# Optimization experiments

Measured on AMD Instinct MI355X. Metric: run time of the kernel, lower is better.

## Reference

```python
import jax, jax.numpy as jnp
import numpy as np

M, T, D, H = 2, 2048, 1024, 16
HD = D // H
SCALE = 1.0 / np.sqrt(D).astype(np.float32)  # original divides by sqrt(emb_dim)


def setup_inputs() -> dict:
    key = jax.random.key(0)
    ks = jax.random.split(key, 8)
    def lin(k):
        kw, kb = jax.random.split(k)
        W = jax.random.normal(kw, (D, D), dtype=jnp.float32) * (1.0 / np.sqrt(D))
        b = jax.random.normal(kb, (D,), dtype=jnp.float32) * 0.01
        return W, b
    Wq, bq = lin(ks[0]); Wk, bk = lin(ks[1]); Wv, bv = lin(ks[2]); Wo, bo = lin(ks[3])
    Q = jax.random.normal(ks[4], (M, T, D), dtype=jnp.float32)
    K = jax.random.normal(ks[5], (M, T, D), dtype=jnp.float32)
    V = jax.random.normal(ks[6], (M, T, D), dtype=jnp.float32)
    mask = jnp.ones((M, 1, 1, T), dtype=jnp.int32)
    return {"Q": Q, "K": K, "V": V, "mask": mask,
            "Wq": Wq, "bq": bq, "Wk": Wk, "bk": bk,
            "Wv": Wv, "bv": bv, "Wo": Wo, "bo": bo}


def reference(Q, K, V, mask, Wq, bq, Wk, bk, Wv, bv, Wo, bo):
    m = Q.shape[0]
    # torch nn.Linear: y = x @ W.T + b
    q = (Q @ Wq.T + bq).reshape(m, -1, H, HD)  # (m, Tq, h, hd)
    k = (K @ Wk.T + bk).reshape(m, -1, H, HD)
    v = (V @ Wv.T + bv).reshape(m, -1, H, HD)
    energy = jnp.einsum('mqhd,mkhd->mhqk', q, k) * SCALE
    if mask is not None:
        energy = jnp.where(mask == 0, jnp.float32(-1e20), energy)
    attn = jax.nn.softmax(energy, axis=3)  # dropout is identity at inference
    out = jnp.einsum('mhqk,mkhd->mqhd', attn, v)  # (m, Tq, h, hd)
    concat = out.reshape(m, -1, H * HD)
    return concat @ Wo.T + bo
```

## Files before the change

kernel.cpp:

```cpp
#include <hip/hip_runtime.h>
#include <cstdint>
#include <cstddef>

#define T_SEQ 2048
#define D_EMB 1024
#define H_HEADS 16
#define MROWS 4096
#define SC2 (0.03125f * 1.44269504f)
#define MASKNEG (-1e30f)

typedef __attribute__((ext_vector_type(8))) short bf16x8;
typedef __attribute__((ext_vector_type(4))) float f32x4;
typedef __attribute__((ext_vector_type(16))) float f32x16;
typedef __attribute__((ext_vector_type(4))) unsigned short us4;

__device__ __forceinline__ unsigned short f2bf(float f) {
  union { float f; uint32_t u; } v; v.f = f;
  uint32_t u = v.u;
  return (unsigned short)((u + 0x7FFFu + ((u >> 16) & 1u)) >> 16);
}

__device__ __forceinline__ uint32_t cvtpk(float lo, float hi) {
  uint32_t r;
  asm("v_cvt_pk_bf16_f32 %0, %1, %2" : "=v"(r) : "v"(lo), "v"(hi));
  return r;
}

__device__ __forceinline__ float fexp2(float x) {
  float r;
  asm("v_exp_f32 %0, %1" : "=v"(r) : "v"(x));
  return r;
}

__device__ __forceinline__ float bf2f(unsigned short u) {
  union { uint32_t u; float f; } v; v.u = ((uint32_t)u) << 16;
  return v.f;
}

__device__ __forceinline__ void gl16(const void* g, void* l) {
  __builtin_amdgcn_global_load_lds(
      (const __attribute__((address_space(1))) unsigned int*)g,
      (__attribute__((address_space(3))) unsigned int*)l, 16, 0, 0);
}

__global__ __launch_bounds__(256) void cvt_all(
    const float* __restrict__ Q, const float* __restrict__ K, const float* __restrict__ V,
    const float* __restrict__ Wq, const float* __restrict__ Wk,
    const float* __restrict__ Wv, const float* __restrict__ Wo,
    unsigned short* __restrict__ Qb, unsigned short* __restrict__ Kb,
    unsigned short* __restrict__ Vb,
    unsigned short* __restrict__ Wqb, unsigned short* __restrict__ Wkb,
    unsigned short* __restrict__ Wvb, unsigned short* __restrict__ Wob) {
  int i = blockIdx.x * 256 + threadIdx.x;
  const float* src;
  unsigned short* dst;
  int j;
  if (i < 3145728) {
    int s = i >> 20;
    j = i & 1048575;
    src = (s == 0) ? Q : (s == 1) ? K : V;
    dst = (s == 0) ? Qb : (s == 1) ? Kb : Vb;
  } else {
    int k = i - 3145728;
    int s = k >> 18;
    j = k & 262143;
    src = (s == 0) ? Wq : (s == 1) ? Wk : (s == 2) ? Wv : Wo;
    dst = (s == 0) ? Wqb : (s == 1) ? Wkb : (s == 2) ? Wvb : Wob;
  }
  float4 f = ((const float4*)src)[j];
  us4 o;
  o[0] = f2bf(f.x); o[1] = f2bf(f.y); o[2] = f2bf(f.z); o[3] = f2bf(f.w);
  ((us4*)dst)[j] = o;
}

__global__ __launch_bounds__(256) void qkv_gemm(
    const unsigned short* __restrict__ Qb, const unsigned short* __restrict__ Kb,
    const unsigned short* __restrict__ Vb,
    const unsigned short* __restrict__ Wqb, const unsigned short* __restrict__ Wkb,
    const unsigned short* __restrict__ Wvb,
    const float* __restrict__ bq, const float* __restrict__ bk, const float* __restrict__ bv,
    unsigned short* __restrict__ qo, unsigned short* __restrict__ ko,
    unsigned short* __restrict__ vto) {
  const int swz = (blockIdx.x & 7) * 192 + (blockIdx.x >> 3);
  const int bx = swz & 15, by = (swz >> 4) & 31, z = swz >> 9;
  const unsigned short* A = (z == 0) ? Qb : (z == 1) ? Kb : Vb;
  const unsigned short* W = (z == 0) ? Wqb : (z == 1) ? Wkb : Wvb;
  const float* bias = (z == 0) ? bq : (z == 1) ? bk : bv;

  __shared__ __align__(16) unsigned short Asm[2][128 * 32];
  __shared__ __align__(16) unsigned short Bsm[2][64 * 32];

  const int tid = threadIdx.x;
  const int lane = tid & 63, w = tid >> 6;
  const int fq = lane >> 4, fr = lane & 15;
  const int brow = by * 128, bcol = bx * 64;
  const int wr = w * 32;

  f32x4 acc[2][4] = {};

#define QKV_STAGE(buf, k0)                                                     \
  {                                                                            \
    _Pragma("unroll") for (int it = 0; it < 2; ++it) {                         \
      int idx = it * 256 + tid;                                                \
      int row = idx >> 2, ce = (idx & 3) * 8;                                  \
      gl16(&A[(size_t)(brow + row) * D_EMB + (k0) + ce],                       \
           (char*)Asm[buf] + idx * 16);                                        \
    }                                                                          \
    {                                                                          \
      int row = tid >> 2, ce = (tid & 3) * 8;                                  \
      gl16(&W[(size_t)(bcol + row) * D_EMB + (k0) + ce],                       \
           (char*)Bsm[buf] + tid * 16);                                        \
    }                                                                          \
  }

#define QKV_COMPUTE(buf)                                                       \
  {                                                                            \
    bf16x8 af[2], bfr[4];                                                      \
    _Pragma("unroll") for (int i = 0; i < 2; ++i)                              \
        af[i] = *(const bf16x8*)((const char*)Asm[buf] +                       \
                                 (wr + i * 16 + fr) * 64 + fq * 16);           \
    _Pragma("unroll") for (int j = 0; j < 4; ++j)                              \
        bfr[j] = *(const bf16x8*)((const char*)Bsm[buf] +                      \
                                  (j * 16 + fr) * 64 + fq * 16);               \
    _Pragma("unroll") for (int i = 0; i < 2; ++i)                              \
        _Pragma("unroll") for (int j = 0; j < 4; ++j)                          \
            acc[i][j] = __builtin_amdgcn_mfma_f32_16x16x32_bf16(               \
                af[i], bfr[j], acc[i][j], 0, 0, 0);                            \
  }

  QKV_STAGE(0, 0);
  __syncthreads();
#pragma unroll 1
  for (int t = 0; t < 32; t += 2) {
    QKV_STAGE(1, (t + 1) * 32);
    QKV_COMPUTE(0);
    __syncthreads();
    if (t + 2 < 32) QKV_STAGE(0, (t + 2) * 32);
    QKV_COMPUTE(1);
    __syncthreads();
  }

#pragma unroll
  for (int i = 0; i < 2; ++i) {
#pragma unroll
    for (int j = 0; j < 4; ++j) {
      int r0 = brow + wr + i * 16 + fq * 4;
      int cc = bcol + j * 16 + fr;
      float bb = bias[cc];
      if (z < 2) {
        unsigned short* O = (z == 0) ? qo : ko;
        float sc = (z == 0) ? SC2 : 1.0f;
#pragma unroll
        for (int q = 0; q < 4; ++q)
          O[(size_t)(r0 + q) * D_EMB + cc] = f2bf((acc[i][j][q] + bb) * sc);
      } else {
        int hh = cc >> 6, dd = cc & 63;
        int mm = r0 >> 11, tt = r0 & 2047;
        us4 pk;
#pragma unroll
        for (int q = 0; q < 4; ++q) pk[q] = f2bf(acc[i][j][q] + bb);
        *(us4*)&vto[((size_t)((mm * H_HEADS + hh) * 64 + dd)) * T_SEQ + tt] = pk;
      }
    }
  }
}

__global__ __launch_bounds__(256) void out_gemm(const unsigned short* __restrict__ Ab,
                                                const unsigned short* __restrict__ Wb,
                                                const float* __restrict__ bias,
                                                float* __restrict__ Out) {
  const int swz = (blockIdx.x & 7) * 64 + (blockIdx.x >> 3);
  const int bx = swz & 15, by = swz >> 4;

  __shared__ __align__(16) unsigned short Asm[2][128 * 32];
  __shared__ __align__(16) unsigned short Bsm[2][64 * 32];
  const int tid = threadIdx.x;
  const int lane = tid & 63, w = tid >> 6;
  const int fq = lane >> 4, fr = lane & 15;
  const int brow = by * 128, bcol = bx * 64;
  const int wr = w * 32;

  f32x4 acc[2][4] = {};

#define OUT_STAGE(buf, k0)                                                     \
  {                                                                            \
    _Pragma("unroll") for (int it = 0; it < 2; ++it) {                         \
      int idx = it * 256 + tid;                                                \
      int row = idx >> 2, ce = (idx & 3) * 8;                                  \
      gl16(&Ab[(size_t)(brow + row) * D_EMB + (k0) + ce],                      \
           (char*)Asm[buf] + idx * 16);                                        \
    }                                                                          \
    {                                                                          \
      int row = tid >> 2, ce = (tid & 3) * 8;                                  \
      gl16(&Wb[(size_t)(bcol + row) * D_EMB + (k0) + ce],                      \
           (char*)Bsm[buf] + tid * 16);                                        \
    }                                                                          \
  }

#define OUT_COMPUTE(buf)                                                       \
  {                                                                            \
    bf16x8 af[2], bfr[4];                                                      \
    _Pragma("unroll") for (int i = 0; i < 2; ++i)                              \
        af[i] = *(const bf16x8*)((const char*)Asm[buf] +                       \
                                 (wr + i * 16 + fr) * 64 + fq * 16);           \
    _Pragma("unroll") for (int j = 0; j < 4; ++j)                              \
        bfr[j] = *(const bf16x8*)((const char*)Bsm[buf] +                      \
                                  (j * 16 + fr) * 64 + fq * 16);               \
    _Pragma("unroll") for (int i = 0; i < 2; ++i)                              \
        _Pragma("unroll") for (int j = 0; j < 4; ++j)                          \
            acc[i][j] = __builtin_amdgcn_mfma_f32_16x16x32_bf16(               \
                af[i], bfr[j], acc[i][j], 0, 0, 0);                            \
  }

  OUT_STAGE(0, 0);
  __syncthreads();
#pragma unroll 1
  for (int t = 0; t < 32; t += 2) {
    OUT_STAGE(1, (t + 1) * 32);
    OUT_COMPUTE(0);
    __syncthreads();
    if (t + 2 < 32) OUT_STAGE(0, (t + 2) * 32);
    OUT_COMPUTE(1);
    __syncthreads();
  }

#pragma unroll
  for (int i = 0; i < 2; ++i)
#pragma unroll
    for (int j = 0; j < 4; ++j) {
      int r0 = brow + wr + i * 16 + fq * 4;
      int cc = bcol + j * 16 + fr;
      float bb = bias[cc];
#pragma unroll
      for (int q = 0; q < 4; ++q)
        Out[(size_t)(r0 + q) * D_EMB + cc] = acc[i][j][q] + bb;
    }
}

__global__ __launch_bounds__(256, 4) void attn_fwd(const unsigned short* __restrict__ qb,
                                                   const unsigned short* __restrict__ kb,
                                                   const unsigned short* __restrict__ vtb,
                                                   const int* __restrict__ maskg,
                                                   unsigned short* __restrict__ opart,
                                                   float* __restrict__ lipart) {
  const int swzb = (blockIdx.x & 7) * 128 + (blockIdx.x >> 3);
  const int qt = swzb & 15, h = (swzb >> 4) & 15, mI = (swzb >> 8) & 1, sp = swzb >> 9;
  const int tid = threadIdx.x;
  const int lane = tid & 63, w = tid >> 6;
  const int lq = lane & 31, h2 = lane >> 5;
  const int xk = (lq & 7) << 4;
  const int vx = (lq & 7) << 4;

  __shared__ __align__(16) unsigned short Ksm[128 * 64];
  __shared__ __align__(16) unsigned short Vsm[64 * 128];
  __shared__ __align__(16) float Msm[128];
  __shared__ int moks[16];

  char* KsmB = (char*)Ksm;
  char* VsmB = (char*)Vsm;

  if (tid < 16) moks[tid] = 1;
  __syncthreads();
  {
    int bad = 0;
    const int4* mg = (const int4*)&maskg[mI * T_SEQ + tid * 8];
    int4 a = mg[0], b = mg[1];
    bad |= (a.x == 0) | (a.y == 0) | (a.z == 0) | (a.w == 0);
    bad |= (b.x == 0) | (b.y == 0) | (b.z == 0) | (b.w == 0);
    if (bad) moks[tid >> 4] = 0;
  }
  __syncthreads();
  int okbits = 0;
#pragma unroll
  for (int i = 0; i < 16; ++i) okbits |= (moks[i] != 0) << i;

  const int qrow = qt * 128 + w * 32 + lq;
  bf16x8 qf[4];
#pragma unroll
  for (int db = 0; db < 4; ++db)
    qf[db] = *(const bf16x8*)&qb[((size_t)(mI * T_SEQ) + qrow) * D_EMB + h * 64 + db * 16 + h2 * 8];

  f32x16 oacc[2] = {};
  float li = 0.f;

  const unsigned short* kpan = kb + (size_t)(mI * T_SEQ) * D_EMB + h * 64;
  const unsigned short* vpan = vtb + (size_t)(mI * H_HEADS + h) * 64 * T_SEQ;

#pragma unroll 1
  for (int t = sp * 8; t < sp * 8 + 8; ++t) {
    const int okv = (okbits >> t) & 1;
    const int k0s = t * 128;
#pragma unroll
    for (int it = 0; it < 4; ++it) {
      int idx = it * 256 + tid;
      int row = idx >> 3;
      int sb = ((idx & 7) * 16) ^ ((row & 7) << 4);
      gl16(kpan + (size_t)(k0s + row) * D_EMB + (sb >> 1), KsmB + idx * 16);
    }
#pragma unroll
    for (int it = 0; it < 4; ++it) {
      int idx = it * 256 + tid;
      int row = idx >> 4;
      int sb = ((idx & 15) * 16) ^ ((row & 7) << 4);
      gl16(vpan + (size_t)row * T_SEQ + k0s + (sb >> 1), VsmB + idx * 16);
    }
    if (!okv && tid < 128)
      Msm[tid] = (maskg[mI * T_SEQ + k0s + tid] == 0) ? MASKNEG : 0.f;
    __syncthreads();

#pragma unroll 1
    for (int kbk = 0; kbk < 4; ++kbk) {
      f32x16 sv = {};
      const char* kr = KsmB + (kbk * 32 + lq) * 128;
#pragma unroll
      for (int db = 0; db < 4; ++db) {
        bf16x8 kf = *(const bf16x8*)(kr + ((db * 32 + h2 * 16) ^ xk));
        sv = __builtin_amdgcn_mfma_f32_32x32x16_bf16(kf, qf[db], sv, 0, 0, 0);
      }
      if (!okv) {
#pragma unroll
        for (int rg = 0; rg < 4; ++rg) {
          f32x4 mk = *(const f32x4*)&Msm[kbk * 32 + rg * 8 + h2 * 4];
          sv[rg * 4 + 0] += mk[0]; sv[rg * 4 + 1] += mk[1];
          sv[rg * 4 + 2] += mk[2]; sv[rg * 4 + 3] += mk[3];
        }
      }
#pragma unroll
      for (int r = 0; r < 16; ++r) sv[r] = fexp2(sv[r]);
      {
        float t0 = (sv[0] + sv[1]) + (sv[2] + sv[3]);
        float t1 = (sv[4] + sv[5]) + (sv[6] + sv[7]);
        float t2 = (sv[8] + sv[9]) + (sv[10] + sv[11]);
        float t3 = (sv[12] + sv[13]) + (sv[14] + sv[15]);
        li += (t0 + t1) + (t2 + t3);
      }
      uint32_t w0 = cvtpk(sv[0], sv[1]), w1 = cvtpk(sv[2], sv[3]);
      uint32_t w2 = cvtpk(sv[4], sv[5]), w3 = cvtpk(sv[6], sv[7]);
      uint32_t w4 = cvtpk(sv[8], sv[9]), w5 = cvtpk(sv[10], sv[11]);
      uint32_t w6 = cvtpk(sv[12], sv[13]), w7 = cvtpk(sv[14], sv[15]);
      uint32_t x0 = __shfl_xor(w0, 32), x1 = __shfl_xor(w1, 32);
      uint32_t x2 = __shfl_xor(w2, 32), x3 = __shfl_xor(w3, 32);
      uint32_t x4 = __shfl_xor(w4, 32), x5 = __shfl_xor(w5, 32);
      uint32_t x6 = __shfl_xor(w6, 32), x7 = __shfl_xor(w7, 32);
      bf16x8 pf[2];
      {
        union { bf16x8 v; uint32_t u[4]; } u_;
        u_.u[0] = h2 ? x2 : w0; u_.u[1] = h2 ? x3 : w1;
        u_.u[2] = h2 ? w2 : x0; u_.u[3] = h2 ? w3 : x1;
        pf[0] = u_.v;
      }
      {
        union { bf16x8 v; uint32_t u[4]; } u_;
        u_.u[0] = h2 ? x6 : w4; u_.u[1] = h2 ? x7 : w5;
        u_.u[2] = h2 ? w6 : x4; u_.u[3] = h2 ? w7 : x5;
        pf[1] = u_.v;
      }
#pragma unroll
      for (int vb = 0; vb < 2; ++vb) {
        const char* vbase = VsmB + (vb * 32 + lq) * 256;
#pragma unroll
        for (int s = 0; s < 2; ++s) {
          bf16x8 vf = *(const bf16x8*)(vbase + ((kbk * 64 + s * 32 + h2 * 16) ^ vx));
          oacc[vb] = __builtin_amdgcn_mfma_f32_32x32x16_bf16(vf, pf[s], oacc[vb], 0, 0, 0);
        }
      }
    }
    __syncthreads();
  }

  li += __shfl_xor(li, 32);

  unsigned short* op = opart + (size_t)sp * ((size_t)MROWS * D_EMB);
  size_t orow = (size_t)(mI * T_SEQ + qrow) * D_EMB + h * 64;
#pragma unroll
  for (int vb = 0; vb < 2; ++vb)
#pragma unroll
    for (int rg = 0; rg < 4; ++rg) {
      uint2 ow;
      ow.x = cvtpk(oacc[vb][rg * 4 + 0], oacc[vb][rg * 4 + 1]);
      ow.y = cvtpk(oacc[vb][rg * 4 + 2], oacc[vb][rg * 4 + 3]);
      *(uint2*)&op[orow + vb * 32 + rg * 8 + h2 * 4] = ow;
    }
  if (h2 == 0)
    lipart[((size_t)sp * MROWS + mI * T_SEQ + qrow) * H_HEADS + h] = li;
}

__global__ __launch_bounds__(256) void combine(const unsigned short* __restrict__ opart,
                                               const float* __restrict__ lipart,
                                               unsigned short* __restrict__ cc) {
  int i = blockIdx.x * 256 + threadIdx.x;
  int row = i >> 7;
  int c8 = i & 127;
  int h = c8 >> 3;
  float l0 = lipart[(size_t)row * H_HEADS + h];
  float l1 = lipart[((size_t)MROWS + row) * H_HEADS + h];
  float inv = 1.f / (l0 + l1);
  size_t off = (size_t)row * D_EMB + c8 * 8;
  us4 a0 = *(const us4*)&opart[off];
  us4 a1 = *(const us4*)&opart[off + 4];
  us4 b0 = *(const us4*)&opart[(size_t)MROWS * D_EMB + off];
  us4 b1 = *(const us4*)&opart[(size_t)MROWS * D_EMB + off + 4];
  uint2 o0, o1;
  o0.x = cvtpk((bf2f(a0[0]) + bf2f(b0[0])) * inv, (bf2f(a0[1]) + bf2f(b0[1])) * inv);
  o0.y = cvtpk((bf2f(a0[2]) + bf2f(b0[2])) * inv, (bf2f(a0[3]) + bf2f(b0[3])) * inv);
  o1.x = cvtpk((bf2f(a1[0]) + bf2f(b1[0])) * inv, (bf2f(a1[1]) + bf2f(b1[1])) * inv);
  o1.y = cvtpk((bf2f(a1[2]) + bf2f(b1[2])) * inv, (bf2f(a1[3]) + bf2f(b1[3])) * inv);
  *(uint2*)&cc[off] = o0;
  *(uint2*)&cc[off + 4] = o1;
}

extern "C" void kernel_launch(void* const* d_in, const int* in_sizes, int n_in,
                              void* d_out, int out_size, void* d_ws, size_t ws_size,
                              hipStream_t stream) {
  const float* Q  = (const float*)d_in[0];
  const float* K  = (const float*)d_in[1];
  const float* V  = (const float*)d_in[2];
  const int* mask = (const int*)d_in[3];
  const float* Wq = (const float*)d_in[4];
  const float* bq = (const float*)d_in[5];
  const float* Wk = (const float*)d_in[6];
  const float* bk = (const float*)d_in[7];
  const float* Wv = (const float*)d_in[8];
  const float* bv = (const float*)d_in[9];
  const float* Wo = (const float*)d_in[10];
  const float* bo = (const float*)d_in[11];

  uint8_t* ws = (uint8_t*)d_ws;
  const size_t MB = 1u << 20;
  unsigned short* Wq_b = (unsigned short*)(ws + 0 * MB);
  unsigned short* Wk_b = (unsigned short*)(ws + 2 * MB);
  unsigned short* Wv_b = (unsigned short*)(ws + 4 * MB);
  unsigned short* Wo_b = (unsigned short*)(ws + 6 * MB);
  unsigned short* q_b  = (unsigned short*)(ws + 8 * MB);
  unsigned short* k_b  = (unsigned short*)(ws + 16 * MB);
  unsigned short* vt_b = (unsigned short*)(ws + 24 * MB);
  unsigned short* Qb    = (unsigned short*)(ws + 32 * MB);
  unsigned short* Kb    = (unsigned short*)(ws + 40 * MB);
  unsigned short* Vb    = (unsigned short*)(ws + 48 * MB);
  unsigned short* opart = (unsigned short*)(ws + 32 * MB);
  unsigned short* cc_b  = (unsigned short*)(ws + 48 * MB);
  float*          lipart = (float*)(ws + 56 * MB);

  cvt_all<<<dim3(16384), dim3(256), 0, stream>>>(Q, K, V, Wq, Wk, Wv, Wo,
                                                 Qb, Kb, Vb, Wq_b, Wk_b, Wv_b, Wo_b);

  qkv_gemm<<<dim3(1536), dim3(256), 0, stream>>>(
      Qb, Kb, Vb, Wq_b, Wk_b, Wv_b, bq, bk, bv, q_b, k_b, vt_b);

  attn_fwd<<<dim3(1024), dim3(256), 0, stream>>>(
      q_b, k_b, vt_b, mask, opart, lipart);

  combine<<<dim3(2048), dim3(256), 0, stream>>>(opart, lipart, cc_b);

  out_gemm<<<dim3(512), dim3(256), 0, stream>>>(
      cc_b, Wo_b, bo, (float*)d_out);
}
```

Before: 139.8 us.

## Parameterize attention KV split count and halve KV tile to 64 keys

The attention kernel now stages 64-key K/V tiles in shared memory instead of 128. The number of KV splits is a runtime parameter, set to 4 when the workspace is at least 64 MB and 2 otherwise, so the grid can grow to 2048 blocks. The combine kernel loops over however many partial outputs and row sums there are, and the workspace buffers are moved to make room. The aim is more parallelism and lower shared-memory use per block, at the cost of more partial-output traffic in the combine step and more barriers per key.

```diff
diff --git a/kernel.cpp b/kernel.cpp
--- a/kernel.cpp
+++ b/kernel.cpp
@@ -242,24 +242,27 @@
                                                    const unsigned short* __restrict__ vtb,
                                                    const int* __restrict__ maskg,
                                                    unsigned short* __restrict__ opart,
-                                                   float* __restrict__ lipart) {
-  const int swzb = (blockIdx.x & 7) * 128 + (blockIdx.x >> 3);
+                                                   float* __restrict__ lipart,
+                                                   int nsp) {
+  const int cpx = gridDim.x >> 3;
+  const int swzb = (blockIdx.x & 7) * cpx + (blockIdx.x >> 3);
   const int qt = swzb & 15, h = (swzb >> 4) & 15, mI = (swzb >> 8) & 1, sp = swzb >> 9;
+  const int ntpb = 32 / nsp;
   const int tid = threadIdx.x;
   const int lane = tid & 63, w = tid >> 6;
   const int lq = lane & 31, h2 = lane >> 5;
   const int xk = (lq & 7) << 4;
   const int vx = (lq & 7) << 4;
 
-  __shared__ __align__(16) unsigned short Ksm[128 * 64];
-  __shared__ __align__(16) unsigned short Vsm[64 * 128];
-  __shared__ __align__(16) float Msm[128];
-  __shared__ int moks[16];
+  __shared__ __align__(16) unsigned short Ksm[64 * 64];
+  __shared__ __align__(16) unsigned short Vsm[64 * 64];
+  __shared__ __align__(16) float Msm[64];
+  __shared__ int moks[32];
 
   char* KsmB = (char*)Ksm;
   char* VsmB = (char*)Vsm;
 
-  if (tid < 16) moks[tid] = 1;
+  if (tid < 32) moks[tid] = 1;
   __syncthreads();
   {
     int bad = 0;
@@ -267,12 +270,12 @@
     int4 a = mg[0], b = mg[1];
     bad |= (a.x == 0) | (a.y == 0) | (a.z == 0) | (a.w == 0);
     bad |= (b.x == 0) | (b.y == 0) | (b.z == 0) | (b.w == 0);
-    if (bad) moks[tid >> 4] = 0;
+    if (bad) moks[tid >> 3] = 0;
   }
   __syncthreads();
-  int okbits = 0;
-#pragma unroll
-  for (int i = 0; i < 16; ++i) okbits |= (moks[i] != 0) << i;
+  uint32_t okbits = 0;
+#pragma unroll
+  for (int i = 0; i < 32; ++i) okbits |= (uint32_t)(moks[i] != 0) << i;
 
   const int qrow = qt * 128 + w * 32 + lq;
   bf16x8 qf[4];
@@ -287,29 +290,29 @@
   const unsigned short* vpan = vtb + (size_t)(mI * H_HEADS + h) * 64 * T_SEQ;
 
 #pragma unroll 1
-  for (int t = sp * 8; t < sp * 8 + 8; ++t) {
+  for (int t = sp * ntpb; t < sp * ntpb + ntpb; ++t) {
     const int okv = (okbits >> t) & 1;
-    const int k0s = t * 128;
-#pragma unroll
-    for (int it = 0; it < 4; ++it) {
+    const int k0s = t * 64;
+#pragma unroll
+    for (int it = 0; it < 2; ++it) {
       int idx = it * 256 + tid;
       int row = idx >> 3;
       int sb = ((idx & 7) * 16) ^ ((row & 7) << 4);
       gl16(kpan + (size_t)(k0s + row) * D_EMB + (sb >> 1), KsmB + idx * 16);
     }
 #pragma unroll
-    for (int it = 0; it < 4; ++it) {
+    for (int it = 0; it < 2; ++it) {
       int idx = it * 256 + tid;
-      int row = idx >> 4;
-      int sb = ((idx & 15) * 16) ^ ((row & 7) << 4);
+      int row = idx >> 3;
+      int sb = ((idx & 7) * 16) ^ ((row & 7) << 4);
       gl16(vpan + (size_t)row * T_SEQ + k0s + (sb >> 1), VsmB + idx * 16);
     }
-    if (!okv && tid < 128)
+    if (!okv && tid < 64)
       Msm[tid] = (maskg[mI * T_SEQ + k0s + tid] == 0) ? MASKNEG : 0.f;
     __syncthreads();
 
 #pragma unroll 1
-    for (int kbk = 0; kbk < 4; ++kbk) {
+    for (int kbk = 0; kbk < 2; ++kbk) {
       f32x16 sv = {};
       const char* kr = KsmB + (kbk * 32 + lq) * 128;
 #pragma unroll
@@ -357,7 +360,7 @@
       }
 #pragma unroll
       for (int vb = 0; vb < 2; ++vb) {
-        const char* vbase = VsmB + (vb * 32 + lq) * 256;
+        const char* vbase = VsmB + (vb * 32 + lq) * 128;
 #pragma unroll
         for (int s = 0; s < 2; ++s) {
           bf16x8 vf = *(const bf16x8*)(vbase + ((kbk * 64 + s * 32 + h2 * 16) ^ vx));
@@ -387,24 +390,30 @@
 
 __global__ __launch_bounds__(256) void combine(const unsigned short* __restrict__ opart,
                                                const float* __restrict__ lipart,
-                                               unsigned short* __restrict__ cc) {
+                                               unsigned short* __restrict__ cc,
+                                               int nsp) {
   int i = blockIdx.x * 256 + threadIdx.x;
   int row = i >> 7;
   int c8 = i & 127;
   int h = c8 >> 3;
-  float l0 = lipart[(size_t)row * H_HEADS + h];
-  float l1 = lipart[((size_t)MROWS + row) * H_HEADS + h];
-  float inv = 1.f / (l0 + l1);
+  float lsum = 0.f;
+  float acc[8] = {};
+#pragma unroll 1
+  for (int s = 0; s < nsp; ++s) {
+    lsum += lipart[((size_t)s * MROWS + row) * H_HEADS + h];
+    size_t off = (size_t)s * MROWS * D_EMB + (size_t)row * D_EMB + c8 * 8;
+    us4 a0 = *(const us4*)&opart[off];
+    us4 a1 = *(const us4*)&opart[off + 4];
+#pragma unroll
+    for (int e = 0; e < 4; ++e) { acc[e] += bf2f(a0[e]); acc[4 + e] += bf2f(a1[e]); }
+  }
+  float inv = 1.f / lsum;
+  uint2 o0, o1;
+  o0.x = cvtpk(acc[0] * inv, acc[1] * inv);
+  o0.y = cvtpk(acc[2] * inv, acc[3] * inv);
+  o1.x = cvtpk(acc[4] * inv, acc[5] * inv);
+  o1.y = cvtpk(acc[6] * inv, acc[7] * inv);
   size_t off = (size_t)row * D_EMB + c8 * 8;
-  us4 a0 = *(const us4*)&opart[off];
-  us4 a1 = *(const us4*)&opart[off + 4];
-  us4 b0 = *(const us4*)&opart[(size_t)MROWS * D_EMB + off];
-  us4 b1 = *(const us4*)&opart[(size_t)MROWS * D_EMB + off + 4];
-  uint2 o0, o1;
-  o0.x = cvtpk((bf2f(a0[0]) + bf2f(b0[0])) * inv, (bf2f(a0[1]) + bf2f(b0[1])) * inv);
-  o0.y = cvtpk((bf2f(a0[2]) + bf2f(b0[2])) * inv, (bf2f(a0[3]) + bf2f(b0[3])) * inv);
-  o1.x = cvtpk((bf2f(a1[0]) + bf2f(b1[0])) * inv, (bf2f(a1[1]) + bf2f(b1[1])) * inv);
-  o1.y = cvtpk((bf2f(a1[2]) + bf2f(b1[2])) * inv, (bf2f(a1[3]) + bf2f(b1[3])) * inv);
   *(uint2*)&cc[off] = o0;
   *(uint2*)&cc[off + 4] = o1;
 }
@@ -438,8 +447,10 @@
   unsigned short* Kb    = (unsigned short*)(ws + 40 * MB);
   unsigned short* Vb    = (unsigned short*)(ws + 48 * MB);
   unsigned short* opart = (unsigned short*)(ws + 32 * MB);
-  unsigned short* cc_b  = (unsigned short*)(ws + 48 * MB);
-  float*          lipart = (float*)(ws + 56 * MB);
+  float*          lipart = (float*)(ws + 0 * MB);
+  unsigned short* cc_b  = (unsigned short*)(ws + 8 * MB);
+
+  const int nsp = (ws_size >= (size_t)64 * MB) ? 4 : 2;
 
   cvt_all<<<dim3(16384), dim3(256), 0, stream>>>(Q, K, V, Wq, Wk, Wv, Wo,
                                                  Qb, Kb, Vb, Wq_b, Wk_b, Wv_b, Wo_b);
@@ -447,10 +458,10 @@
   qkv_gemm<<<dim3(1536), dim3(256), 0, stream>>>(
       Qb, Kb, Vb, Wq_b, Wk_b, Wv_b, bq, bk, bv, q_b, k_b, vt_b);
 
-  attn_fwd<<<dim3(1024), dim3(256), 0, stream>>>(
-      q_b, k_b, vt_b, mask, opart, lipart);
-
-  combine<<<dim3(2048), dim3(256), 0, stream>>>(opart, lipart, cc_b);
+  attn_fwd<<<dim3(512 * nsp), dim3(256), 0, stream>>>(
+      q_b, k_b, vt_b, mask, opart, lipart, nsp);
+
+  combine<<<dim3(2048), dim3(256), 0, stream>>>(opart, lipart, cc_b, nsp);
 
   out_gemm<<<dim3(512), dim3(256), 0, stream>>>(
       cc_b, Wo_b, bo, (float*)d_out);
```

Result: slower. 146.2 us (+4.5%).
